# Performance work log

Hardware: AMD Instinct MI355X
Metric: run time of the kernel (lower is better)

The kernel has to match this reference:

```python
import jax, jax.numpy as jnp
import numpy as np

NEG = -1e9
LRELU_ALPHA = 0.2  # tf.nn.leaky_relu default


def setup_inputs() -> dict:
    key = jax.random.key(0)
    k = jax.random.split(key, 6)
    B, N, F_in, F_out = 1, 8192, 256, 64
    x = jax.random.normal(k[0], (B, N, F_in), dtype=jnp.float32)
    # sparse adjacency as additive bias: ~32 neighbors/node on average
    u = jax.random.uniform(k[1], (B, N, N), dtype=jnp.float32)
    adj = jnp.where(u < 32.0 / N, 0.0, NEG).astype(jnp.float32)
    W = jax.random.normal(k[2], (F_in, F_out), dtype=jnp.float32) * (1.0 / np.sqrt(F_in))
    a1 = jax.random.normal(k[3], (F_out, 1), dtype=jnp.float32) * (1.0 / np.sqrt(F_out))
    a2 = jax.random.normal(k[4], (F_out, 1), dtype=jnp.float32) * (1.0 / np.sqrt(F_out))
    b1 = jnp.zeros((1,), dtype=jnp.float32)
    b2 = jnp.zeros((1,), dtype=jnp.float32)
    bias = jnp.zeros((F_out,), dtype=jnp.float32)
    return {"x": x, "adj": adj, "W": W, "a1": a1, "b1": b1, "a2": a2, "b2": b2, "bias": bias}


def reference(x, adj, W, a1, b1, a2, b2, bias):
    # conv1 (kernel_size=1, no bias) == per-node linear projection
    fts = jnp.einsum('bnf,fo->bno', x, W)            # [B, N, F_out]
    f1 = jnp.einsum('bno,oi->bni', fts, a1) + b1     # [B, N, 1]
    f2 = jnp.einsum('bno,oi->bni', fts, a2) + b2     # [B, N, 1]
    logits = f1 + jnp.swapaxes(f2, 1, 2)             # [B, N, N] additive scores
    scores = jax.nn.leaky_relu(logits, LRELU_ALPHA) + adj
    coefs = jax.nn.softmax(scores, axis=-1)          # [B, N, N]
    vals = jnp.einsum('bnm,bmo->bno', coefs, fts) + bias
    return jax.nn.elu(vals)
```

## Files before the change

### kernel.cpp

```cpp
#include <hip/hip_runtime.h>
#include <cstdint>

#define N_NODES 8192
#define F_IN    256
#define F_OUT   64
#define ALPHA   0.2f
#define CAP     512

__global__ __launch_bounds__(256) void k_proj(const float* __restrict__ x,
                                              const float* __restrict__ W,
                                              const float* __restrict__ a1,
                                              const float* __restrict__ b1,
                                              const float* __restrict__ a2,
                                              const float* __restrict__ b2,
                                              float* __restrict__ fts,
                                              float* __restrict__ f1,
                                              float* __restrict__ f2) {
    __shared__ __align__(16) float ws[64][F_OUT];
    const int t = threadIdx.x, lane = t & 63, w = t >> 6;
    const int rowA = blockIdx.x * 8 + w * 2;
    const int rowB = rowA + 1;

    const float4* xqA = (const float4*)(x + (size_t)rowA * F_IN);
    const float4* xqB = (const float4*)(x + (size_t)rowB * F_IN);
    float accA = 0.f, accB = 0.f;

    for (int kc = 0; kc < 4; ++kc) {
        if (kc) __syncthreads();
        {
            const float4* Wt = (const float4*)(W + (size_t)kc * 64 * F_OUT);
            float4* S = (float4*)&ws[0][0];
            S[t]       = Wt[t];
            S[t + 256] = Wt[t + 256];
            S[t + 512] = Wt[t + 512];
            S[t + 768] = Wt[t + 768];
        }
        __syncthreads();
        #pragma unroll
        for (int q = 0; q < 16; ++q) {
            const float4 xa = xqA[kc * 16 + q];
            const float4 xb = xqB[kc * 16 + q];
            const float w0 = ws[q*4+0][lane];
            const float w1 = ws[q*4+1][lane];
            const float w2 = ws[q*4+2][lane];
            const float w3 = ws[q*4+3][lane];
            accA += xa.x*w0 + xa.y*w1 + xa.z*w2 + xa.w*w3;
            accB += xb.x*w0 + xb.y*w1 + xb.z*w2 + xb.w*w3;
        }
    }
    fts[(size_t)rowA * F_OUT + lane] = accA;
    fts[(size_t)rowB * F_OUT + lane] = accB;

    const float u1 = a1[lane], u2 = a2[lane];
    float sA1 = accA * u1, sA2 = accA * u2;
    float sB1 = accB * u1, sB2 = accB * u2;
    #pragma unroll
    for (int off = 32; off >= 1; off >>= 1) {
        sA1 += __shfl_xor(sA1, off, 64);
        sA2 += __shfl_xor(sA2, off, 64);
        sB1 += __shfl_xor(sB1, off, 64);
        sB2 += __shfl_xor(sB2, off, 64);
    }
    if (lane == 0) {
        const float bb1 = b1[0], bb2 = b2[0];
        f1[rowA] = sA1 + bb1;  f2[rowA] = sA2 + bb2;
        f1[rowB] = sB1 + bb1;  f2[rowB] = sB2 + bb2;
    }
}

__global__ __launch_bounds__(256) void k_attn(const float* __restrict__ adj,
                                              const float* __restrict__ fts,
                                              const float* __restrict__ f1,
                                              const float* __restrict__ f2,
                                              const float* __restrict__ bias,
                                              float* __restrict__ out) {
    __shared__ int   nbr[CAP];
    __shared__ float sl[CAP];
    __shared__ int   cnt;
    __shared__ float wred[4], wsum[4];
    __shared__ __align__(16) float wacc[4][F_OUT];

    const int row = blockIdx.x, t = threadIdx.x;
    const int lane = t & 63, w = t >> 6;
    if (t == 0) cnt = 0;
    __syncthreads();

    const float4* arow = (const float4*)(adj + (size_t)row * N_NODES);

    #define PUSH(v, jj) if ((v) > -0.5f) { int p = atomicAdd(&cnt, 1); if (p < CAP) nbr[p] = (jj); }
    #pragma unroll
    for (int b = 0; b < 2; ++b) {
        const int q0 = (b * 4 + 0) * 256 + t;
        const int q1 = (b * 4 + 1) * 256 + t;
        const int q2 = (b * 4 + 2) * 256 + t;
        const int q3 = (b * 4 + 3) * 256 + t;
        const float4 a0 = arow[q0];
        const float4 a1v = arow[q1];
        const float4 a2v = arow[q2];
        const float4 a3v = arow[q3];
        PUSH(a0.x, 4*q0+0) PUSH(a0.y, 4*q0+1) PUSH(a0.z, 4*q0+2) PUSH(a0.w, 4*q0+3)
        PUSH(a1v.x,4*q1+0) PUSH(a1v.y,4*q1+1) PUSH(a1v.z,4*q1+2) PUSH(a1v.w,4*q1+3)
        PUSH(a2v.x,4*q2+0) PUSH(a2v.y,4*q2+1) PUSH(a2v.z,4*q2+2) PUSH(a2v.w,4*q2+3)
        PUSH(a3v.x,4*q3+0) PUSH(a3v.y,4*q3+1) PUSH(a3v.z,4*q3+2) PUSH(a3v.w,4*q3+3)
    }
    #undef PUSH
    __syncthreads();

    const int n = (cnt < CAP) ? cnt : CAP;
    const float f1r = f1[row];

    float m = -3.0e38f;
    for (int k = t; k < n; k += 256) {
        const int j = nbr[k];
        const float lg = f1r + f2[j];
        const float l  = fmaxf(lg, ALPHA * lg);
        sl[k] = l;
        m = fmaxf(m, l);
    }
    #pragma unroll
    for (int off = 32; off >= 1; off >>= 1)
        m = fmaxf(m, __shfl_xor(m, off, 64));
    if (lane == 0) wred[w] = m;
    __syncthreads();
    const float M = fmaxf(fmaxf(wred[0], wred[1]), fmaxf(wred[2], wred[3]));

    float acc = 0.f, psum = 0.f;
    for (int k = w; k < n; k += 4) {
        const float p = __expf(sl[k] - M);
        psum += p;
        acc += p * fts[(size_t)nbr[k] * F_OUT + lane];
    }
    if (lane == 0) wsum[w] = psum;
    wacc[w][lane] = acc;
    __syncthreads();

    if (w == 0) {
        const float den = wsum[0] + wsum[1] + wsum[2] + wsum[3];
        const float tot = wacc[0][lane] + wacc[1][lane] + wacc[2][lane] + wacc[3][lane];
        const float v = tot / den + bias[lane];
        out[(size_t)row * F_OUT + lane] = (v > 0.f) ? v : expm1f(v);
    }
}

extern "C" void kernel_launch(void* const* d_in, const int* in_sizes, int n_in,
                              void* d_out, int out_size, void* d_ws, size_t ws_size,
                              hipStream_t stream) {
    const float* x    = (const float*)d_in[0];
    const float* adj  = (const float*)d_in[1];
    const float* W    = (const float*)d_in[2];
    const float* a1   = (const float*)d_in[3];
    const float* b1   = (const float*)d_in[4];
    const float* a2   = (const float*)d_in[5];
    const float* b2   = (const float*)d_in[6];
    const float* bias = (const float*)d_in[7];
    float* out = (float*)d_out;

    float* fts = (float*)d_ws;
    float* f1  = fts + (size_t)N_NODES * F_OUT;
    float* f2  = f1 + N_NODES;

    k_proj<<<N_NODES / 8, 256, 0, stream>>>(x, W, a1, b1, a2, b2, fts, f1, f2);
    k_attn<<<N_NODES, 256, 0, stream>>>(adj, fts, f1, f2, bias, out);
}
```

Measured before the change: 395.2 us.

## Split attention into grid-wide adjacency scan and wave-per-row gather kernels

Replaces the per-row attention kernel with two kernels. A flat grid-stride scan streams the whole adjacency matrix and appends neighbor indices to per-row global lists through global atomics, with the counters zeroed inside the projection kernel. A gather kernel then assigns one wavefront per row, keeps logits in registers and broadcasts weights and indices with shuffles, so no shared memory or block barriers are needed. The neighbor cap drops from 512 to 256, which could silently truncate unusually dense rows, and the extra launch adds a global round trip for the neighbor lists.

```diff
diff --git a/kernel.cpp b/kernel.cpp
--- a/kernel.cpp
+++ b/kernel.cpp
@@ -5,7 +5,7 @@
 #define F_IN    256
 #define F_OUT   64
 #define ALPHA   0.2f
-#define CAP     512
+#define CAP     256
 
 __global__ __launch_bounds__(256) void k_proj(const float* __restrict__ x,
                                               const float* __restrict__ W,
@@ -15,9 +15,13 @@
                                               const float* __restrict__ b2,
                                               float* __restrict__ fts,
                                               float* __restrict__ f1,
-                                              float* __restrict__ f2) {
+                                              float* __restrict__ f2,
+                                              int* __restrict__ cnt) {
     __shared__ __align__(16) float ws[64][F_OUT];
     const int t = threadIdx.x, lane = t & 63, w = t >> 6;
+
+    if (blockIdx.x < 32) cnt[blockIdx.x * 256 + t] = 0;
+
     const int rowA = blockIdx.x * 8 + w * 2;
     const int rowB = rowA + 1;
 
@@ -68,78 +72,97 @@
     }
 }
 
-__global__ __launch_bounds__(256) void k_attn(const float* __restrict__ adj,
-                                              const float* __restrict__ fts,
-                                              const float* __restrict__ f1,
-                                              const float* __restrict__ f2,
-                                              const float* __restrict__ bias,
-                                              float* __restrict__ out) {
-    __shared__ int   nbr[CAP];
-    __shared__ float sl[CAP];
-    __shared__ int   cnt;
-    __shared__ float wred[4], wsum[4];
-    __shared__ __align__(16) float wacc[4][F_OUT];
+__global__ __launch_bounds__(256) void k_scan(const float* __restrict__ adj,
+                                              int* __restrict__ cnt,
+                                              int* __restrict__ list) {
+    const int S = gridDim.x * 256;
+    int q = blockIdx.x * 256 + threadIdx.x;
+    const float4* A = (const float4*)adj;
 
-    const int row = blockIdx.x, t = threadIdx.x;
-    const int lane = t & 63, w = t >> 6;
-    if (t == 0) cnt = 0;
-    __syncthreads();
+    #pragma unroll 1
+    for (int it = 0; it < 8; ++it) {
+        const float4 v0 = A[q];
+        const float4 v1 = A[q + S];
+        const float4 v2 = A[q + 2 * S];
+        const float4 v3 = A[q + 3 * S];
 
-    const float4* arow = (const float4*)(adj + (size_t)row * N_NODES);
+        #define PROC(v, qq)                                                     \
+        {                                                                       \
+            const int e = (qq) << 2;                                            \
+            const int r = e >> 13;                                              \
+            const int c = e & (N_NODES - 1);                                    \
+            if ((v).x > -0.5f) { int p = atomicAdd(&cnt[r], 1); if (p < CAP) list[(r << 8) + p] = c;     } \
+            if ((v).y > -0.5f) { int p = atomicAdd(&cnt[r], 1); if (p < CAP) list[(r << 8) + p] = c + 1; } \
+            if ((v).z > -0.5f) { int p = atomicAdd(&cnt[r], 1); if (p < CAP) list[(r << 8) + p] = c + 2; } \
+            if ((v).w > -0.5f) { int p = atomicAdd(&cnt[r], 1); if (p < CAP) list[(r << 8) + p] = c + 3; } \
+        }
+        PROC(v0, q) PROC(v1, q + S) PROC(v2, q + 2 * S) PROC(v3, q + 3 * S)
+        #undef PROC
+        q += 4 * S;
+    }
+}
 
-    #define PUSH(v, jj) if ((v) > -0.5f) { int p = atomicAdd(&cnt, 1); if (p < CAP) nbr[p] = (jj); }
-    #pragma unroll
-    for (int b = 0; b < 2; ++b) {
-        const int q0 = (b * 4 + 0) * 256 + t;
-        const int q1 = (b * 4 + 1) * 256 + t;
-        const int q2 = (b * 4 + 2) * 256 + t;
-        const int q3 = (b * 4 + 3) * 256 + t;
-        const float4 a0 = arow[q0];
-        const float4 a1v = arow[q1];
-        const float4 a2v = arow[q2];
-        const float4 a3v = arow[q3];
-        PUSH(a0.x, 4*q0+0) PUSH(a0.y, 4*q0+1) PUSH(a0.z, 4*q0+2) PUSH(a0.w, 4*q0+3)
-        PUSH(a1v.x,4*q1+0) PUSH(a1v.y,4*q1+1) PUSH(a1v.z,4*q1+2) PUSH(a1v.w,4*q1+3)
-        PUSH(a2v.x,4*q2+0) PUSH(a2v.y,4*q2+1) PUSH(a2v.z,4*q2+2) PUSH(a2v.w,4*q2+3)
-        PUSH(a3v.x,4*q3+0) PUSH(a3v.y,4*q3+1) PUSH(a3v.z,4*q3+2) PUSH(a3v.w,4*q3+3)
-    }
-    #undef PUSH
-    __syncthreads();
+__global__ __launch_bounds__(256) void k_gather(const int* __restrict__ cnt,
+                                                const int* __restrict__ list,
+                                                const float* __restrict__ fts,
+                                                const float* __restrict__ f1,
+                                                const float* __restrict__ f2,
+                                                const float* __restrict__ bias,
+                                                float* __restrict__ out) {
+    const int lane = threadIdx.x & 63, w = threadIdx.x >> 6;
+    const int row  = blockIdx.x * 4 + w;
 
-    const int n = (cnt < CAP) ? cnt : CAP;
+    int n = cnt[row];
+    n = (n < CAP) ? n : CAP;
+    const int* lst = list + (row << 8);
     const float f1r = f1[row];
 
-    float m = -3.0e38f;
-    for (int k = t; k < n; k += 256) {
-        const int j = nbr[k];
-        const float lg = f1r + f2[j];
-        const float l  = fmaxf(lg, ALPHA * lg);
-        sl[k] = l;
-        m = fmaxf(m, l);
-    }
+    float l0 = -3.0e38f, l1 = -3.0e38f, l2 = -3.0e38f, l3 = -3.0e38f;
+    int   j0 = 0, j1 = 0, j2 = 0, j3 = 0;
+    if (lane < n)       { j0 = lst[lane];       const float g = f1r + f2[j0]; l0 = fmaxf(g, ALPHA * g); }
+    if (lane + 64 < n)  { j1 = lst[lane + 64];  const float g = f1r + f2[j1]; l1 = fmaxf(g, ALPHA * g); }
+    if (lane + 128 < n) { j2 = lst[lane + 128]; const float g = f1r + f2[j2]; l2 = fmaxf(g, ALPHA * g); }
+    if (lane + 192 < n) { j3 = lst[lane + 192]; const float g = f1r + f2[j3]; l3 = fmaxf(g, ALPHA * g); }
+
+    float m = fmaxf(fmaxf(l0, l1), fmaxf(l2, l3));
     #pragma unroll
     for (int off = 32; off >= 1; off >>= 1)
         m = fmaxf(m, __shfl_xor(m, off, 64));
-    if (lane == 0) wred[w] = m;
-    __syncthreads();
-    const float M = fmaxf(fmaxf(wred[0], wred[1]), fmaxf(wred[2], wred[3]));
 
-    float acc = 0.f, psum = 0.f;
-    for (int k = w; k < n; k += 4) {
-        const float p = __expf(sl[k] - M);
-        psum += p;
-        acc += p * fts[(size_t)nbr[k] * F_OUT + lane];
+    const float p0 = __expf(l0 - m);
+    const float p1 = __expf(l1 - m);
+    const float p2 = __expf(l2 - m);
+    const float p3 = __expf(l3 - m);
+
+    float den = (p0 + p1) + (p2 + p3);
+    #pragma unroll
+    for (int off = 32; off >= 1; off >>= 1)
+        den += __shfl_xor(den, off, 64);
+
+    float acc = 0.f;
+    {
+        const int nb = (n < 64) ? n : 64;
+        for (int k = 0; k < nb; ++k)
+            acc += __shfl(p0, k, 64) * fts[(size_t)__shfl(j0, k, 64) * F_OUT + lane];
     }
-    if (lane == 0) wsum[w] = psum;
-    wacc[w][lane] = acc;
-    __syncthreads();
+    if (n > 64) {
+        const int nb = (n - 64 < 64) ? n - 64 : 64;
+        for (int k = 0; k < nb; ++k)
+            acc += __shfl(p1, k, 64) * fts[(size_t)__shfl(j1, k, 64) * F_OUT + lane];
+    }
+    if (n > 128) {
+        const int nb = (n - 128 < 64) ? n - 128 : 64;
+        for (int k = 0; k < nb; ++k)
+            acc += __shfl(p2, k, 64) * fts[(size_t)__shfl(j2, k, 64) * F_OUT + lane];
+    }
+    if (n > 192) {
+        const int nb = (n - 192 < 64) ? n - 192 : 64;
+        for (int k = 0; k < nb; ++k)
+            acc += __shfl(p3, k, 64) * fts[(size_t)__shfl(j3, k, 64) * F_OUT + lane];
+    }
 
-    if (w == 0) {
-        const float den = wsum[0] + wsum[1] + wsum[2] + wsum[3];
-        const float tot = wacc[0][lane] + wacc[1][lane] + wacc[2][lane] + wacc[3][lane];
-        const float v = tot / den + bias[lane];
-        out[(size_t)row * F_OUT + lane] = (v > 0.f) ? v : expm1f(v);
-    }
+    const float v = acc / den + bias[lane];
+    out[(size_t)row * F_OUT + lane] = (v > 0.f) ? v : expm1f(v);
 }
 
 extern "C" void kernel_launch(void* const* d_in, const int* in_sizes, int n_in,
@@ -158,7 +181,10 @@
     float* fts = (float*)d_ws;
     float* f1  = fts + (size_t)N_NODES * F_OUT;
     float* f2  = f1 + N_NODES;
+    int*   cnt = (int*)(f2 + N_NODES);
+    int*   lst = cnt + N_NODES;
 
-    k_proj<<<N_NODES / 8, 256, 0, stream>>>(x, W, a1, b1, a2, b2, fts, f1, f2);
-    k_attn<<<N_NODES, 256, 0, stream>>>(adj, fts, f1, f2, bias, out);
+    k_proj  <<<N_NODES / 8, 256, 0, stream>>>(x, W, a1, b1, a2, b2, fts, f1, f2, cnt);
+    k_scan  <<<2048,        256, 0, stream>>>(adj, cnt, lst);
+    k_gather<<<N_NODES / 4, 256, 0, stream>>>(cnt, lst, fts, f1, f2, bias, out);
 }
```

Result: slower. 422.5 us (+6.9%).
